# Kernel tuning notes

Hardware: AMD Instinct MI355X
Metric: run time of the kernel (lower is better)

Reference implementation:

```python
import jax, jax.numpy as jnp
import numpy as np

CENTER_X = 0.5  # image_center_x default from module signature


def setup_inputs() -> dict:
    key = jax.random.key(0)
    k1, k2 = jax.random.split(key)
    B, N = 256, 512
    predicted_keypoints = jax.random.uniform(k1, (B, N, 2), dtype=jnp.float32)
    # classes in [-2, 6): negatives are invalid, 0..2 are symmetric classes, 3..5 non-symmetric
    keypoint_classes = jax.random.randint(k2, (B, N), -2, 6, dtype=jnp.int32)
    return {"predicted_keypoints": predicted_keypoints, "keypoint_classes": keypoint_classes}


def reference(predicted_keypoints, keypoint_classes):
    # predicted_keypoints: [B, N, 2], keypoint_classes: [B, N]
    # Original loops over i<j among valid points; a pair contributes iff
    # class_i == class_j and class in {0,1,2} (the symmetric-pairs set).
    # Per-pair loss (right_x - (2*cx - left_x))^2 + (right_y - left_y)^2
    # = (x_i + x_j - 2*cx)^2 + (y_i - y_j)^2, which is symmetric in (i, j),
    # so the left/right assignment is irrelevant to the math.
    c = keypoint_classes
    x = predicted_keypoints[..., 0]  # [B, N]
    y = predicted_keypoints[..., 1]  # [B, N]
    N = c.shape[1]

    sym = (c[:, :, None] == c[:, None, :]) & (c[:, :, None] >= 0) & (c[:, :, None] <= 2)
    tri = jnp.triu(jnp.ones((N, N), dtype=bool), k=1)  # i < j
    mask = sym & tri  # [B, N, N]

    pair_loss = (x[:, :, None] + x[:, None, :] - 2.0 * CENTER_X) ** 2 \
              + (y[:, :, None] - y[:, None, :]) ** 2  # [B, N, N]

    total = jnp.sum(jnp.where(mask, pair_loss, 0.0))
    count = jnp.sum(mask).astype(pair_loss.dtype)
    return total / jnp.maximum(count, 1.0)
```

## Files before the change

### kernel.cpp

```cpp
#include <hip/hip_runtime.h>

#define BATCH 256
#define NPTS  512
#define CENTER_X 0.5f

__global__ __launch_bounds__(NPTS) void sym_batch_reduce(
    const float* __restrict__ kp,
    const int* __restrict__ cls,
    float* __restrict__ ws) {
  const int b = blockIdx.x;
  const int t = threadIdx.x;

  const float2 p = ((const float2*)kp)[b * NPTS + t];
  const int c = cls[b * NPTS + t];
  const float u = p.x - CENTER_X;
  const float y = p.y;

  float v[15];
#pragma unroll
  for (int k = 0; k < 3; ++k) {
    const float sel = (c == k) ? 1.0f : 0.0f;
    v[5 * k + 0] = sel * u;
    v[5 * k + 1] = sel * u * u;
    v[5 * k + 2] = sel * y;
    v[5 * k + 3] = sel * y * y;
    v[5 * k + 4] = sel;
  }

#pragma unroll
  for (int off = 32; off >= 1; off >>= 1) {
#pragma unroll
    for (int i = 0; i < 15; ++i) v[i] += __shfl_down(v[i], off, 64);
  }

  __shared__ float lds[NPTS / 64][15];
  const int wave = t >> 6;
  const int lane = t & 63;
  if (lane == 0) {
#pragma unroll
    for (int i = 0; i < 15; ++i) lds[wave][i] = v[i];
  }
  __syncthreads();

  if (t == 0) {
    float total = 0.0f, count = 0.0f;
#pragma unroll
    for (int k = 0; k < 3; ++k) {
      float su = 0.f, su2 = 0.f, sy = 0.f, sy2 = 0.f, m = 0.f;
#pragma unroll
      for (int w = 0; w < NPTS / 64; ++w) {
        su  += lds[w][5 * k + 0];
        su2 += lds[w][5 * k + 1];
        sy  += lds[w][5 * k + 2];
        sy2 += lds[w][5 * k + 3];
        m   += lds[w][5 * k + 4];
      }
      total += (m - 2.0f) * su2 + su * su + m * sy2 - sy * sy;
      count += 0.5f * m * (m - 1.0f);
    }
    ws[b] = total;
    ws[BATCH + b] = count;
  }
}

__global__ __launch_bounds__(BATCH) void sym_final_reduce(
    const float* __restrict__ ws, float* __restrict__ out) {
  const int t = threadIdx.x;
  float total = ws[t];
  float count = ws[BATCH + t];

#pragma unroll
  for (int off = 32; off >= 1; off >>= 1) {
    total += __shfl_down(total, off, 64);
    count += __shfl_down(count, off, 64);
  }

  __shared__ float lt[BATCH / 64], lc[BATCH / 64];
  const int wave = t >> 6;
  const int lane = t & 63;
  if (lane == 0) { lt[wave] = total; lc[wave] = count; }
  __syncthreads();

  if (t == 0) {
    float T = 0.f, C = 0.f;
#pragma unroll
    for (int w = 0; w < BATCH / 64; ++w) { T += lt[w]; C += lc[w]; }
    out[0] = T / fmaxf(C, 1.0f);
  }
}

extern "C" void kernel_launch(void* const* d_in, const int* in_sizes, int n_in,
                              void* d_out, int out_size, void* d_ws, size_t ws_size,
                              hipStream_t stream) {
  const float* kp = (const float*)d_in[0];
  const int* cls = (const int*)d_in[1];
  float* out = (float*)d_out;
  float* ws = (float*)d_ws;

  sym_batch_reduce<<<BATCH, NPTS, 0, stream>>>(kp, cls, ws);
  sym_final_reduce<<<1, BATCH, 0, stream>>>(ws, out);
}
```

Measured before the change: 58.83 us.

## Fuse batch and final reductions via last-block ticket, halve threads per block

Merges the two-kernel reduction into one kernel. Each block publishes its partial sums and takes an atomic ticket, and the last block to finish performs the final cross-batch reduction. Block size drops to 256 threads, each handling two points, which cuts shuffle-reduction work per point. A memset is added to reset the ticket, so there is still an extra stream operation, and the last block adds a serial tail.

```diff
diff --git a/kernel.cpp b/kernel.cpp
--- a/kernel.cpp
+++ b/kernel.cpp
@@ -2,29 +2,42 @@
 
 #define BATCH 256
 #define NPTS  512
+#define TPB   256
+#define PPT   (NPTS / TPB)
 #define CENTER_X 0.5f
 
-__global__ __launch_bounds__(NPTS) void sym_batch_reduce(
+__global__ __launch_bounds__(TPB) void sym_fused(
     const float* __restrict__ kp,
     const int* __restrict__ cls,
-    float* __restrict__ ws) {
+    float* __restrict__ out,
+    int* __restrict__ ticket,
+    float* __restrict__ totals,
+    float* __restrict__ counts) {
   const int b = blockIdx.x;
   const int t = threadIdx.x;
-
-  const float2 p = ((const float2*)kp)[b * NPTS + t];
-  const int c = cls[b * NPTS + t];
-  const float u = p.x - CENTER_X;
-  const float y = p.y;
+  const int wave = t >> 6;
+  const int lane = t & 63;
 
   float v[15];
 #pragma unroll
-  for (int k = 0; k < 3; ++k) {
-    const float sel = (c == k) ? 1.0f : 0.0f;
-    v[5 * k + 0] = sel * u;
-    v[5 * k + 1] = sel * u * u;
-    v[5 * k + 2] = sel * y;
-    v[5 * k + 3] = sel * y * y;
-    v[5 * k + 4] = sel;
+  for (int i = 0; i < 15; ++i) v[i] = 0.0f;
+
+#pragma unroll
+  for (int p = 0; p < PPT; ++p) {
+    const int idx = b * NPTS + p * TPB + t;
+    const float2 q = ((const float2*)kp)[idx];
+    const int c = cls[idx];
+    const float u = q.x - CENTER_X;
+    const float y = q.y;
+#pragma unroll
+    for (int k = 0; k < 3; ++k) {
+      const float sel = (c == k) ? 1.0f : 0.0f;
+      v[5 * k + 0] += sel * u;
+      v[5 * k + 1] += sel * u * u;
+      v[5 * k + 2] += sel * y;
+      v[5 * k + 3] += sel * y * y;
+      v[5 * k + 4] += sel;
+    }
   }
 
 #pragma unroll
@@ -33,9 +46,8 @@
     for (int i = 0; i < 15; ++i) v[i] += __shfl_down(v[i], off, 64);
   }
 
-  __shared__ float lds[NPTS / 64][15];
-  const int wave = t >> 6;
-  const int lane = t & 63;
+  __shared__ float lds[TPB / 64][15];
+  __shared__ int is_last;
   if (lane == 0) {
 #pragma unroll
     for (int i = 0; i < 15; ++i) lds[wave][i] = v[i];
@@ -48,7 +60,7 @@
     for (int k = 0; k < 3; ++k) {
       float su = 0.f, su2 = 0.f, sy = 0.f, sy2 = 0.f, m = 0.f;
 #pragma unroll
-      for (int w = 0; w < NPTS / 64; ++w) {
+      for (int w = 0; w < TPB / 64; ++w) {
         su  += lds[w][5 * k + 0];
         su2 += lds[w][5 * k + 1];
         sy  += lds[w][5 * k + 2];
@@ -58,34 +70,32 @@
       total += (m - 2.0f) * su2 + su * su + m * sy2 - sy * sy;
       count += 0.5f * m * (m - 1.0f);
     }
-    ws[b] = total;
-    ws[BATCH + b] = count;
+    __hip_atomic_store(&totals[b], total, __ATOMIC_RELAXED, __HIP_MEMORY_SCOPE_AGENT);
+    __hip_atomic_store(&counts[b], count, __ATOMIC_RELAXED, __HIP_MEMORY_SCOPE_AGENT);
+    __threadfence();
+    const int old = __hip_atomic_fetch_add(ticket, 1, __ATOMIC_ACQ_REL,
+                                           __HIP_MEMORY_SCOPE_AGENT);
+    is_last = (old == (int)gridDim.x - 1);
   }
-}
-
-__global__ __launch_bounds__(BATCH) void sym_final_reduce(
-    const float* __restrict__ ws, float* __restrict__ out) {
-  const int t = threadIdx.x;
-  float total = ws[t];
-  float count = ws[BATCH + t];
-
-#pragma unroll
-  for (int off = 32; off >= 1; off >>= 1) {
-    total += __shfl_down(total, off, 64);
-    count += __shfl_down(count, off, 64);
-  }
-
-  __shared__ float lt[BATCH / 64], lc[BATCH / 64];
-  const int wave = t >> 6;
-  const int lane = t & 63;
-  if (lane == 0) { lt[wave] = total; lc[wave] = count; }
   __syncthreads();
 
-  if (t == 0) {
-    float T = 0.f, C = 0.f;
+  if (is_last) {
+    float T = __hip_atomic_load(&totals[t], __ATOMIC_RELAXED, __HIP_MEMORY_SCOPE_AGENT);
+    float C = __hip_atomic_load(&counts[t], __ATOMIC_RELAXED, __HIP_MEMORY_SCOPE_AGENT);
 #pragma unroll
-    for (int w = 0; w < BATCH / 64; ++w) { T += lt[w]; C += lc[w]; }
-    out[0] = T / fmaxf(C, 1.0f);
+    for (int off = 32; off >= 1; off >>= 1) {
+      T += __shfl_down(T, off, 64);
+      C += __shfl_down(C, off, 64);
+    }
+    __shared__ float lt[TPB / 64], lc[TPB / 64];
+    if (lane == 0) { lt[wave] = T; lc[wave] = C; }
+    __syncthreads();
+    if (t == 0) {
+      float Ts = 0.f, Cs = 0.f;
+#pragma unroll
+      for (int w = 0; w < TPB / 64; ++w) { Ts += lt[w]; Cs += lc[w]; }
+      out[0] = Ts / fmaxf(Cs, 1.0f);
+    }
   }
 }
 
@@ -95,8 +105,11 @@
   const float* kp = (const float*)d_in[0];
   const int* cls = (const int*)d_in[1];
   float* out = (float*)d_out;
-  float* ws = (float*)d_ws;
 
-  sym_batch_reduce<<<BATCH, NPTS, 0, stream>>>(kp, cls, ws);
-  sym_final_reduce<<<1, BATCH, 0, stream>>>(ws, out);
+  int* ticket = (int*)d_ws;
+  float* totals = (float*)d_ws + 32;
+  float* counts = totals + BATCH;
+
+  hipMemsetAsync(d_ws, 0, 4, stream);
+  sym_fused<<<BATCH, TPB, 0, stream>>>(kp, cls, out, ticket, totals, counts);
 }
```

Result: slower. 65.18 us (+10.8%).
